# Kernel tuning notes

Hardware: AMD Instinct MI355X
Metric: run time of the kernel (lower is better)

The kernel has to match this reference:

```python
import jax, jax.numpy as jnp
import numpy as np

N_STATE = 64
SEQ_L = 4096
BATCH, HCH = 16, 512
DT_MIN, DT_MAX = 0.001, 0.1


def _make_DPLR_HiPPO(N):
    # HiPPO-LegS matrix and its NPLR -> DPLR decomposition (annotated-s4).
    P = np.sqrt(1 + 2 * np.arange(N))
    A = P[:, None] * P[None, :]
    A = np.tril(A) - np.diag(np.arange(N))
    nhippo = -A
    p = 0.5 * np.sqrt(2 * np.arange(1, N + 1) + 1.0)
    q = 2 * p
    S = nhippo + p[:, None] * q[None, :]
    Lambda, V = np.linalg.eig(S)
    Vc = V.conj().T
    p_t = Vc @ p
    q_t = Vc @ q.conj()
    return Lambda, p_t, q_t, Vc


def _ri(z):
    return np.stack([z.real, z.imag], axis=-1).astype(np.float32)


def setup_inputs() -> dict:
    key = jax.random.key(0)
    k_u, k_ct, k_b, k_d, k_ls = jax.random.split(key, 5)
    Lambda, p, q, Vc = _make_DPLR_HiPPO(N_STATE)
    u = jax.random.normal(k_u, (BATCH, HCH, SEQ_L), dtype=jnp.float32)
    # lecun_normal params (fan_in = N)
    Ct_ri = jax.random.normal(k_ct, (1, N_STATE, 2), dtype=jnp.float32) / np.sqrt(N_STATE)
    Bp = jax.random.normal(k_b, (N_STATE, 1), dtype=jnp.float32) / np.sqrt(N_STATE)
    D = jax.random.uniform(k_d, (1,), dtype=jnp.float32)
    log_step = jax.random.uniform(
        k_ls, (1,), dtype=jnp.float32,
        minval=np.log(DT_MIN), maxval=np.log(DT_MAX))
    return {
        "u": u,
        "Lambda_ri": jnp.asarray(_ri(Lambda)),
        "p_ri": jnp.asarray(_ri(p)),
        "q_ri": jnp.asarray(_ri(q)),
        "Vc_ri": jnp.asarray(_ri(Vc)),
        "Ct_ri": Ct_ri,
        "Bp": Bp,
        "D": D,
        "log_step": log_step,
    }


def _cplx(x_ri):
    return x_ri[..., 0] + 1j * x_ri[..., 1]


def _s4_kernel(Lambda, p, q, B, Ct, step, L):
    # DPLR generating function evaluated at the L roots of unity (K_gen_DPLR
    # + conv_from_gen), vectorized over frequencies.
    Omega = jnp.exp((-2j * jnp.pi) * (jnp.arange(L) / L))          # (L,)
    g = (2.0 / step) * ((1.0 - Omega) / (1.0 + Omega))             # (L,)
    c = 2.0 / (1.0 + Omega)                                        # (L,)
    denom = g[:, None] - Lambda[None, :]                           # (L, N)
    cauchy = lambda v: (v[None, :] / denom).sum(-1)                # (L,)
    k00 = cauchy(Ct.conj() * B)
    k01 = cauchy(Ct.conj() * p)
    k10 = cauchy(q.conj() * B)
    k11 = cauchy(q.conj() * p)
    at_roots = c * (k00 - k01 * (1.0 / (1.0 + k11)) * k10)
    return jnp.fft.ifft(at_roots, L).real                          # (L,)


def reference(u, Lambda_ri, p_ri, q_ri, Vc_ri, Ct_ri, Bp, D, log_step):
    L = u.shape[-1]
    Lambda = _cplx(Lambda_ri)
    p = _cplx(p_ri)
    q = _cplx(q_ri)
    Vc = _cplx(Vc_ri)
    Ct = _cplx(Ct_ri).reshape(-1)                  # (N,)
    B = (Vc @ Bp.astype(Vc.dtype)).reshape(-1)     # (N,) complex
    step = jnp.exp(log_step)[0]
    K = _s4_kernel(Lambda, p, q, B, Ct, step, L).astype(u.dtype)   # (L,)
    # non-circular convolution via zero-padded FFT along the last axis
    n = 2 * L
    y = jnp.fft.irfft(jnp.fft.rfft(u, n=n) * jnp.fft.rfft(K, n=n), n=n)[..., :L]
    return y + D[0] * u
```

## Files before the change

### kernel.cpp

```cpp
#include <hip/hip_runtime.h>
#include <math.h>


#define SEQ_L 4096
#define NFFT  8192
#define NST   64
#define NROWS 8192
#define TWO_PI 6.28318530717958647692f

typedef float2 cf;

__device__ __forceinline__ cf cmul(cf a, cf b){ return make_float2(a.x*b.x - a.y*b.y, a.x*b.y + a.y*b.x); }
__device__ __forceinline__ cf cadd(cf a, cf b){ return make_float2(a.x+b.x, a.y+b.y); }
__device__ __forceinline__ cf csub(cf a, cf b){ return make_float2(a.x-b.x, a.y-b.y); }
__device__ __forceinline__ double2 dcmul(double2 a, double2 b) {
  return make_double2(a.x*b.x - a.y*b.y, a.x*b.y + a.y*b.x);
}
__device__ __forceinline__ int sw(int p){ return p ^ ((p >> 4) & 15); }

template<int S>
__device__ __forceinline__ void r4(cf& a0, cf& a1, cf& a2, cf& a3){
  cf t0 = cadd(a0,a2), t1 = csub(a0,a2);
  cf t2 = cadd(a1,a3), t3 = csub(a1,a3);
  cf w = (S < 0) ? make_float2(t3.y, -t3.x) : make_float2(-t3.y, t3.x);
  a0 = cadd(t0,t2); a2 = csub(t0,t2);
  a1 = cadd(t1,w);  a3 = csub(t1,w);
}

template<int S, bool ZHI>
__device__ __forceinline__ void dft8(cf x[8]){
  const float C = 0.70710678118654752f;
  cf e0,e1,e2,e3,o0,o1,o2,o3;
  if (ZHI) {
    cf w  = (S<0)? make_float2(x[2].y,-x[2].x) : make_float2(-x[2].y,x[2].x);
    e0 = cadd(x[0],x[2]); e2 = csub(x[0],x[2]);
    e1 = cadd(x[0],w);    e3 = csub(x[0],w);
    cf w2 = (S<0)? make_float2(x[3].y,-x[3].x) : make_float2(-x[3].y,x[3].x);
    o0 = cadd(x[1],x[3]); o2 = csub(x[1],x[3]);
    o1 = cadd(x[1],w2);   o3 = csub(x[1],w2);
  } else {
    cf a0=x[0],a1=x[2],a2=x[4],a3=x[6];
    r4<S>(a0,a1,a2,a3);  e0=a0;e1=a1;e2=a2;e3=a3;
    cf b0=x[1],b1=x[3],b2=x[5],b3=x[7];
    r4<S>(b0,b1,b2,b3);  o0=b0;o1=b1;o2=b2;o3=b3;
  }
  x[0] = cadd(e0,o0); x[4] = csub(e0,o0);
  cf t1 = (S<0)? make_float2(C*(o1.x+o1.y), C*(o1.y-o1.x))
               : make_float2(C*(o1.x-o1.y), C*(o1.x+o1.y));
  x[1] = cadd(e1,t1); x[5] = csub(e1,t1);
  cf t2 = (S<0)? make_float2(o2.y,-o2.x) : make_float2(-o2.y,o2.x);
  x[2] = cadd(e2,t2); x[6] = csub(e2,t2);
  cf t3 = (S<0)? make_float2(C*(o3.y-o3.x), -C*(o3.x+o3.y))
               : make_float2(-C*(o3.x+o3.y), C*(o3.x-o3.y));
  x[3] = cadd(e3,t3); x[7] = csub(e3,t3);
}

__device__ __forceinline__ void chain8(cf x[8], float th){
  float sn, cs; __sincosf(th, &sn, &cs);
  cf w = make_float2(cs, sn), wk = w;
  x[1] = cmul(x[1], wk);
  #pragma unroll
  for (int k = 2; k < 8; ++k) { wk = cmul(wk, w); x[k] = cmul(x[k], wk); }
}

__device__ __forceinline__ constexpr float c16t(int d){
  return (d==1)?0.92387953251128675613f:(d==2)?0.70710678118654752440f:
         (d==3)?0.38268343236508977173f:(d==4)?0.f:
         (d==5)?-0.38268343236508977173f:(d==6)?-0.70710678118654752440f:
         -0.92387953251128675613f;
}
__device__ __forceinline__ constexpr float s16t(int d){
  return (d==1)?0.38268343236508977173f:(d==2)?0.70710678118654752440f:
         (d==3)?0.92387953251128675613f:(d==4)?1.f:
         (d==5)?0.92387953251128675613f:(d==6)?0.70710678118654752440f:
         0.38268343236508977173f;
}
template<int S>
__device__ __forceinline__ void tw16(cf x[8], int t000){
  #pragma unroll
  for (int d = 1; d < 8; ++d) {
    float ce = t000 ? c16t(d) : 1.f;
    float se = t000 ? ((S < 0) ? -s16t(d) : s16t(d)) : 0.f;
    cf a = x[d];
    x[d] = make_float2(a.x*ce - a.y*se, a.x*se + a.y*ce);
  }
}

__device__ __forceinline__ void r2_shfl(cf x[8], int tid){
  const float sgn = (tid & 1) ? -1.f : 1.f;
  #pragma unroll
  for (int k = 0; k < 8; ++k) {
    float ox = __shfl_xor(x[k].x, 1, 64);
    float oy = __shfl_xor(x[k].y, 1, 64);
    x[k].x = ox + sgn * x[k].x;
    x[k].y = oy + sgn * x[k].y;
  }
}

template<bool ZHI>
__device__ __forceinline__ void fwd_all(cf x[8], cf* lds, int tid){
  int a1 = tid >> 7, t0 = tid & 127, t00 = tid & 15;
  int b2 = (tid >> 4) & 7, c3 = (tid >> 1) & 7, t000 = tid & 1;
  dft8<-1, ZHI>(x);
  chain8(x, -TWO_PI * (float)tid / (float)NFFT);
  #pragma unroll
  for (int a = 0; a < 8; ++a) lds[sw(a*1024 + tid)] = x[a];
  __syncthreads();
  #pragma unroll
  for (int r = 0; r < 8; ++r) x[r] = lds[sw(a1*1024 + t0 + 128*r)];
  dft8<-1, false>(x);
  chain8(x, -TWO_PI * (float)t0 / 1024.f);
  __syncthreads();
  #pragma unroll
  for (int b = 0; b < 8; ++b) lds[sw(a1*1024 + b*128 + t0)] = x[b];
  __syncthreads();
  #pragma unroll
  for (int r = 0; r < 8; ++r) x[r] = lds[sw(a1*1024 + b2*128 + t00 + 16*r)];
  dft8<-1, false>(x);
  chain8(x, -TWO_PI * (float)t00 / 128.f);
  __syncthreads();
  #pragma unroll
  for (int c = 0; c < 8; ++c) lds[sw(a1*1024 + b2*128 + c*16 + t00)] = x[c];
  __syncthreads();
  #pragma unroll
  for (int r = 0; r < 8; ++r) x[r] = lds[sw(a1*1024 + b2*128 + c3*16 + t000 + 2*r)];
  dft8<-1, false>(x);
  tw16<-1>(x, t000);
  r2_shfl(x, tid);
}

__device__ __forceinline__ void inv_all(cf x[8], cf* lds, int tid){
  int a1 = tid >> 7, t0 = tid & 127, t00 = tid & 15;
  int b2 = (tid >> 4) & 7, c3 = (tid >> 1) & 7, t000 = tid & 1;
  r2_shfl(x, tid);
  tw16<1>(x, t000);
  dft8<1, false>(x);
  __syncthreads();
  #pragma unroll
  for (int r = 0; r < 8; ++r) lds[sw(a1*1024 + b2*128 + c3*16 + t000 + 2*r)] = x[r];
  __syncthreads();
  #pragma unroll
  for (int c = 0; c < 8; ++c) x[c] = lds[sw(a1*1024 + b2*128 + c*16 + t00)];
  chain8(x, TWO_PI * (float)t00 / 128.f);
  dft8<1, false>(x);
  __syncthreads();
  #pragma unroll
  for (int r = 0; r < 8; ++r) lds[sw(a1*1024 + b2*128 + t00 + 16*r)] = x[r];
  __syncthreads();
  #pragma unroll
  for (int b = 0; b < 8; ++b) x[b] = lds[sw(a1*1024 + b*128 + t0)];
  chain8(x, TWO_PI * (float)t0 / 1024.f);
  dft8<1, false>(x);
  __syncthreads();
  #pragma unroll
  for (int r = 0; r < 8; ++r) lds[sw(a1*1024 + t0 + 128*r)] = x[r];
  __syncthreads();
  #pragma unroll
  for (int a = 0; a < 8; ++a) x[a] = lds[sw(a*1024 + tid)];
  chain8(x, TWO_PI * (float)tid / (float)NFFT);
  dft8<1, false>(x);
}

__global__ __launch_bounds__(256) void k_at(
    const float* __restrict__ Lam_ri, const float* __restrict__ p_ri,
    const float* __restrict__ q_ri,  const float* __restrict__ Vc_ri,
    const float* __restrict__ Ct_ri, const float* __restrict__ Bp,
    const float* __restrict__ log_step, float2* __restrict__ atroots) {
  __shared__ double2 lam[NST], ctB[NST], ctp[NST], qB[NST], qp[NST];
  __shared__ double stepd;
  int tx = threadIdx.x;
  if (tx < NST) {
    int n = tx;
    double lr = Lam_ri[2*n], li = Lam_ri[2*n+1];
    double pr = p_ri[2*n],  pi = p_ri[2*n+1];
    double qr = q_ri[2*n],  qi = q_ri[2*n+1];
    double cr = Ct_ri[2*n], ci = Ct_ri[2*n+1];
    double br = 0.0, bi = 0.0;
    for (int m = 0; m < NST; ++m) {
      double b = (double)Bp[m];
      br += (double)Vc_ri[2*(n*NST+m)]   * b;
      bi += (double)Vc_ri[2*(n*NST+m)+1] * b;
    }
    lam[n] = make_double2(lr, li);
    ctB[n] = make_double2(cr*br + ci*bi, cr*bi - ci*br);
    ctp[n] = make_double2(cr*pr + ci*pi, cr*pi - ci*pr);
    qB[n]  = make_double2(qr*br + qi*bi, qr*bi - qi*br);
    qp[n]  = make_double2(qr*pr + qi*pi, qr*pi - qi*pr);
  }
  if (tx == 0) stepd = exp((double)log_step[0]);
  __syncthreads();
  int l = blockIdx.x * 256 + tx;
  double ang = -2.0 * M_PI * (double)l / (double)SEQ_L;
  double sn, cs;
  sincos(ang, &sn, &cs);
  double2 onem = make_double2(1.0 - cs, -sn);
  double2 onep = make_double2(1.0 + cs,  sn);
  double den = onep.x*onep.x + onep.y*onep.y;
  double2 ip = make_double2(onep.x/den, -onep.y/den);
  double2 g  = dcmul(onem, ip);
  double tw = 2.0 / stepd;
  g.x *= tw; g.y *= tw;
  double2 cc = make_double2(2.0*ip.x, 2.0*ip.y);
  double2 k00 = make_double2(0,0), k01 = make_double2(0,0);
  double2 k10 = make_double2(0,0), k11 = make_double2(0,0);
  for (int n = 0; n < NST; ++n) {
    double2 L = lam[n];
    double2 d = make_double2(g.x - L.x, g.y - L.y);
    double dd = d.x*d.x + d.y*d.y;
    double2 inv = make_double2(d.x/dd, -d.y/dd);
    double2 v;
    v = ctB[n]; k00.x += v.x*inv.x - v.y*inv.y; k00.y += v.x*inv.y + v.y*inv.x;
    v = ctp[n]; k01.x += v.x*inv.x - v.y*inv.y; k01.y += v.x*inv.y + v.y*inv.x;
    v = qB[n];  k10.x += v.x*inv.x - v.y*inv.y; k10.y += v.x*inv.y + v.y*inv.x;
    v = qp[n];  k11.x += v.x*inv.x - v.y*inv.y; k11.y += v.x*inv.y + v.y*inv.x;
  }
  double2 k11p = make_double2(1.0 + k11.x, k11.y);
  double2 num  = dcmul(k01, k10);
  double dd2 = k11p.x*k11p.x + k11p.y*k11p.y;
  double2 t = make_double2((num.x*k11p.x + num.y*k11p.y)/dd2,
                           (num.y*k11p.x - num.x*k11p.y)/dd2);
  double2 inner = make_double2(k00.x - t.x, k00.y - t.y);
  double2 at = dcmul(cc, inner);
  atroots[l] = make_float2((float)at.x, (float)at.y);
}

__global__ __launch_bounds__(512) void k_kt(const float2* __restrict__ atroots,
                                            float* __restrict__ Kt) {
  int gid  = blockIdx.x * 512 + threadIdx.x;
  int t    = gid >> 6;
  int lane = gid & 63;
  float acc = 0.f;
  for (int l = lane; l < SEQ_L; l += 64) {
    int ph = (l * t) & (SEQ_L - 1);
    float a = (float)ph * (TWO_PI / (float)SEQ_L);
    float sn, cs; __sincosf(a, &sn, &cs);
    float2 v = atroots[l];
    acc += v.x*cs - v.y*sn;
  }
  for (int off = 32; off > 0; off >>= 1) acc += __shfl_down(acc, off, 64);
  if (lane == 0) Kt[t] = acc * (1.0f / (float)SEQ_L);
}

__global__ __launch_bounds__(1024) void k_kf(const float* __restrict__ Kt,
                                             cf* __restrict__ kf) {
  __shared__ cf lds[NFFT];
  int tid = threadIdx.x;
  cf x[8];
  #pragma unroll
  for (int m = 0; m < 4; ++m) x[m] = make_float2(Kt[tid + 1024*m], 0.f);
  #pragma unroll
  for (int m = 4; m < 8; ++m) x[m] = make_float2(0.f, 0.f);
  fwd_all<true>(x, lds, tid);
  const float s = 1.f / (float)NFFT;
  #pragma unroll
  for (int d = 0; d < 8; ++d)
    kf[tid*8 + d] = make_float2(x[d].x * s, x[d].y * s);
}

__global__ __launch_bounds__(1024, 4) void k_conv(const float* __restrict__ u,
                                                  const cf* __restrict__ kf,
                                                  const float* __restrict__ Dp,
                                                  float* __restrict__ out) {
  __shared__ cf lds[NFFT];
  int tid = threadIdx.x;
  size_t row0 = (size_t)blockIdx.x * 2;
  const float* ru0 = u + row0 * SEQ_L;
  const float* ru1 = ru0 + SEQ_L;
  cf x[8];
  #pragma unroll
  for (int m = 0; m < 4; ++m) {
    int n = tid + 1024*m;
    x[m] = make_float2(ru0[n], ru1[n]);
  }
  #pragma unroll
  for (int m = 4; m < 8; ++m) x[m] = make_float2(0.f, 0.f);

  fwd_all<true>(x, lds, tid);

  const float4* kf4 = (const float4*)kf + (size_t)tid * 4;
  #pragma unroll
  for (int k = 0; k < 4; ++k) {
    float4 kk = kf4[k];
    x[2*k]   = cmul(x[2*k],   make_float2(kk.x, kk.y));
    x[2*k+1] = cmul(x[2*k+1], make_float2(kk.z, kk.w));
  }

  inv_all(x, lds, tid);

  float Dv = Dp[0];
  float* o0 = out + row0 * SEQ_L;
  float* o1 = o0 + SEQ_L;
  #pragma unroll
  for (int m = 0; m < 4; ++m) {
    int n = tid + 1024*m;
    o0[n] = x[m].x + Dv * ru0[n];
    o1[n] = x[m].y + Dv * ru1[n];
  }
}

extern "C" void kernel_launch(void* const* d_in, const int* in_sizes, int n_in,
                              void* d_out, int out_size, void* d_ws, size_t ws_size,
                              hipStream_t stream) {
  const float* u      = (const float*)d_in[0];
  const float* Lam_ri = (const float*)d_in[1];
  const float* p_ri   = (const float*)d_in[2];
  const float* q_ri   = (const float*)d_in[3];
  const float* Vc_ri  = (const float*)d_in[4];
  const float* Ct_ri  = (const float*)d_in[5];
  const float* Bp     = (const float*)d_in[6];
  const float* Dp     = (const float*)d_in[7];
  const float* ls     = (const float*)d_in[8];

  char* ws = (char*)d_ws;
  float2* atroots = (float2*)(ws);
  float*  Kt      = (float*) (ws + 32768);
  cf*     kf      = (cf*)    (ws + 49152);

  k_at<<<dim3(SEQ_L/256), dim3(256), 0, stream>>>(Lam_ri, p_ri, q_ri, Vc_ri, Ct_ri, Bp, ls, atroots);
  k_kt<<<dim3(512), dim3(512), 0, stream>>>(atroots, Kt);
  k_kf<<<dim3(1), dim3(1024), 0, stream>>>(Kt, kf);
  k_conv<<<dim3(NROWS/2), dim3(1024), 0, stream>>>(u, kf, Dp, (float*)d_out);
}
```

Baseline: 204.3 us.

## Convolve each real row via a half-length complex FFT with split post-processing

Replaces the two-rows-packed 8192-point complex FFT convolution with a per-row real-FFT trick. Each real row of 4096 samples is packed as 2048... actually as a 4096-point complex sequence, and the multiply is done in the half-spectrum domain using conjugate-pair (k, M-k) coefficients alpha/beta precomputed in new small kernels. The kernel FFT spectrum is built from even bins taken directly from atroots and odd bins from a direct DFT, which removes the single-block k_kf FFT. The FFT stages now use 512 threads with 8 blocks per CU and new LDS swizzles, and the last inverse radix-8 computes only the needed half. This adds an extra LDS round-trip for the mirrored bins and several tiny kernel launches.

```diff
diff --git a/kernel.cpp b/kernel.cpp
--- a/kernel.cpp
+++ b/kernel.cpp
@@ -3,6 +3,7 @@
 
 
 #define SEQ_L 4096
+#define M4    4096
 #define NFFT  8192
 #define NST   64
 #define NROWS 8192
@@ -16,7 +17,10 @@
 __device__ __forceinline__ double2 dcmul(double2 a, double2 b) {
   return make_double2(a.x*b.x - a.y*b.y, a.x*b.y + a.y*b.x);
 }
-__device__ __forceinline__ int sw(int p){ return p ^ ((p >> 4) & 15); }
+
+__device__ __forceinline__ int s2f(int i){ return i ^ (((i >> 6) & 1) << 3); }
+__device__ __forceinline__ int s3f(int i){ return i ^ ((i >> 6) & 7) ^ (((i >> 6) & 1) << 3); }
+__device__ __forceinline__ int smf(int i){ return i ^ ((i >> 6) & 7); }
 
 template<int S>
 __device__ __forceinline__ void r4(cf& a0, cf& a1, cf& a2, cf& a3){
@@ -27,7 +31,7 @@
   a1 = cadd(t1,w);  a3 = csub(t1,w);
 }
 
-template<int S, bool ZHI>
+template<int S, bool ZHI, bool LO4=false>
 __device__ __forceinline__ void dft8(cf x[8]){
   const float C = 0.70710678118654752f;
   cf e0,e1,e2,e3,o0,o1,o2,o3;
@@ -44,121 +48,29 @@
     cf b0=x[1],b1=x[3],b2=x[5],b3=x[7];
     r4<S>(b0,b1,b2,b3);  o0=b0;o1=b1;o2=b2;o3=b3;
   }
-  x[0] = cadd(e0,o0); x[4] = csub(e0,o0);
+  x[0] = cadd(e0,o0); if (!LO4) x[4] = csub(e0,o0);
   cf t1 = (S<0)? make_float2(C*(o1.x+o1.y), C*(o1.y-o1.x))
                : make_float2(C*(o1.x-o1.y), C*(o1.x+o1.y));
-  x[1] = cadd(e1,t1); x[5] = csub(e1,t1);
+  x[1] = cadd(e1,t1); if (!LO4) x[5] = csub(e1,t1);
   cf t2 = (S<0)? make_float2(o2.y,-o2.x) : make_float2(-o2.y,o2.x);
-  x[2] = cadd(e2,t2); x[6] = csub(e2,t2);
+  x[2] = cadd(e2,t2); if (!LO4) x[6] = csub(e2,t2);
   cf t3 = (S<0)? make_float2(C*(o3.y-o3.x), -C*(o3.x+o3.y))
                : make_float2(-C*(o3.x+o3.y), C*(o3.x-o3.y));
-  x[3] = cadd(e3,t3); x[7] = csub(e3,t3);
+  x[3] = cadd(e3,t3); if (!LO4) x[7] = csub(e3,t3);
 }
 
 __device__ __forceinline__ void chain8(cf x[8], float th){
   float sn, cs; __sincosf(th, &sn, &cs);
-  cf w = make_float2(cs, sn), wk = w;
-  x[1] = cmul(x[1], wk);
-  #pragma unroll
-  for (int k = 2; k < 8; ++k) { wk = cmul(wk, w); x[k] = cmul(x[k], wk); }
-}
-
-__device__ __forceinline__ constexpr float c16t(int d){
-  return (d==1)?0.92387953251128675613f:(d==2)?0.70710678118654752440f:
-         (d==3)?0.38268343236508977173f:(d==4)?0.f:
-         (d==5)?-0.38268343236508977173f:(d==6)?-0.70710678118654752440f:
-         -0.92387953251128675613f;
-}
-__device__ __forceinline__ constexpr float s16t(int d){
-  return (d==1)?0.38268343236508977173f:(d==2)?0.70710678118654752440f:
-         (d==3)?0.92387953251128675613f:(d==4)?1.f:
-         (d==5)?0.92387953251128675613f:(d==6)?0.70710678118654752440f:
-         0.38268343236508977173f;
-}
-template<int S>
-__device__ __forceinline__ void tw16(cf x[8], int t000){
-  #pragma unroll
-  for (int d = 1; d < 8; ++d) {
-    float ce = t000 ? c16t(d) : 1.f;
-    float se = t000 ? ((S < 0) ? -s16t(d) : s16t(d)) : 0.f;
-    cf a = x[d];
-    x[d] = make_float2(a.x*ce - a.y*se, a.x*se + a.y*ce);
-  }
-}
-
-__device__ __forceinline__ void r2_shfl(cf x[8], int tid){
-  const float sgn = (tid & 1) ? -1.f : 1.f;
-  #pragma unroll
-  for (int k = 0; k < 8; ++k) {
-    float ox = __shfl_xor(x[k].x, 1, 64);
-    float oy = __shfl_xor(x[k].y, 1, 64);
-    x[k].x = ox + sgn * x[k].x;
-    x[k].y = oy + sgn * x[k].y;
-  }
-}
-
-template<bool ZHI>
-__device__ __forceinline__ void fwd_all(cf x[8], cf* lds, int tid){
-  int a1 = tid >> 7, t0 = tid & 127, t00 = tid & 15;
-  int b2 = (tid >> 4) & 7, c3 = (tid >> 1) & 7, t000 = tid & 1;
-  dft8<-1, ZHI>(x);
-  chain8(x, -TWO_PI * (float)tid / (float)NFFT);
-  #pragma unroll
-  for (int a = 0; a < 8; ++a) lds[sw(a*1024 + tid)] = x[a];
-  __syncthreads();
-  #pragma unroll
-  for (int r = 0; r < 8; ++r) x[r] = lds[sw(a1*1024 + t0 + 128*r)];
-  dft8<-1, false>(x);
-  chain8(x, -TWO_PI * (float)t0 / 1024.f);
-  __syncthreads();
-  #pragma unroll
-  for (int b = 0; b < 8; ++b) lds[sw(a1*1024 + b*128 + t0)] = x[b];
-  __syncthreads();
-  #pragma unroll
-  for (int r = 0; r < 8; ++r) x[r] = lds[sw(a1*1024 + b2*128 + t00 + 16*r)];
-  dft8<-1, false>(x);
-  chain8(x, -TWO_PI * (float)t00 / 128.f);
-  __syncthreads();
-  #pragma unroll
-  for (int c = 0; c < 8; ++c) lds[sw(a1*1024 + b2*128 + c*16 + t00)] = x[c];
-  __syncthreads();
-  #pragma unroll
-  for (int r = 0; r < 8; ++r) x[r] = lds[sw(a1*1024 + b2*128 + c3*16 + t000 + 2*r)];
-  dft8<-1, false>(x);
-  tw16<-1>(x, t000);
-  r2_shfl(x, tid);
-}
-
-__device__ __forceinline__ void inv_all(cf x[8], cf* lds, int tid){
-  int a1 = tid >> 7, t0 = tid & 127, t00 = tid & 15;
-  int b2 = (tid >> 4) & 7, c3 = (tid >> 1) & 7, t000 = tid & 1;
-  r2_shfl(x, tid);
-  tw16<1>(x, t000);
-  dft8<1, false>(x);
-  __syncthreads();
-  #pragma unroll
-  for (int r = 0; r < 8; ++r) lds[sw(a1*1024 + b2*128 + c3*16 + t000 + 2*r)] = x[r];
-  __syncthreads();
-  #pragma unroll
-  for (int c = 0; c < 8; ++c) x[c] = lds[sw(a1*1024 + b2*128 + c*16 + t00)];
-  chain8(x, TWO_PI * (float)t00 / 128.f);
-  dft8<1, false>(x);
-  __syncthreads();
-  #pragma unroll
-  for (int r = 0; r < 8; ++r) lds[sw(a1*1024 + b2*128 + t00 + 16*r)] = x[r];
-  __syncthreads();
-  #pragma unroll
-  for (int b = 0; b < 8; ++b) x[b] = lds[sw(a1*1024 + b*128 + t0)];
-  chain8(x, TWO_PI * (float)t0 / 1024.f);
-  dft8<1, false>(x);
-  __syncthreads();
-  #pragma unroll
-  for (int r = 0; r < 8; ++r) lds[sw(a1*1024 + t0 + 128*r)] = x[r];
-  __syncthreads();
-  #pragma unroll
-  for (int a = 0; a < 8; ++a) x[a] = lds[sw(a*1024 + tid)];
-  chain8(x, TWO_PI * (float)tid / (float)NFFT);
-  dft8<1, false>(x);
+  cf w1 = make_float2(cs, sn);
+  cf w2 = cmul(w1, w1);
+  cf w3 = cmul(w2, w1);
+  cf w4 = cmul(w2, w2);
+  cf w5 = cmul(w3, w2);
+  cf w6 = cmul(w3, w3);
+  cf w7 = cmul(w4, w3);
+  x[1] = cmul(x[1], w1); x[2] = cmul(x[2], w2); x[3] = cmul(x[3], w3);
+  x[4] = cmul(x[4], w4); x[5] = cmul(x[5], w5); x[6] = cmul(x[6], w6);
+  x[7] = cmul(x[7], w7);
 }
 
 __global__ __launch_bounds__(256) void k_at(
@@ -241,60 +153,151 @@
   if (lane == 0) Kt[t] = acc * (1.0f / (float)SEQ_L);
 }
 
-__global__ __launch_bounds__(1024) void k_kf(const float* __restrict__ Kt,
-                                             cf* __restrict__ kf) {
-  __shared__ cf lds[NFFT];
-  int tid = threadIdx.x;
+__global__ __launch_bounds__(256) void k_geven(const float2* __restrict__ atroots,
+                                               float2* __restrict__ G) {
+  int l = blockIdx.x * 256 + threadIdx.x;
+  if (l > 2048) return;
+  float2 a = atroots[l];
+  float2 b = atroots[(M4 - l) & (M4 - 1)];
+  G[2*l] = make_float2(0.5f*(a.x + b.x), 0.5f*(a.y - b.y));
+}
+
+__global__ __launch_bounds__(512) void k_godd(const float* __restrict__ Kt,
+                                              float2* __restrict__ G) {
+  int gid  = blockIdx.x * 512 + threadIdx.x;
+  int w    = gid >> 6;
+  int k    = 2*w + 1;
+  int lane = gid & 63;
+  float ar = 0.f, ai = 0.f;
+  for (int t = lane; t < SEQ_L; t += 64) {
+    int ph = (k * t) & (NFFT - 1);
+    float a = (float)ph * (-TWO_PI / (float)NFFT);
+    float sn, cs; __sincosf(a, &sn, &cs);
+    float kv = Kt[t];
+    ar += kv * cs; ai += kv * sn;
+  }
+  for (int off = 32; off > 0; off >>= 1) {
+    ar += __shfl_down(ar, off, 64);
+    ai += __shfl_down(ai, off, 64);
+  }
+  if (lane == 0) G[k] = make_float2(ar, ai);
+}
+
+__global__ __launch_bounds__(256) void k_ab(const float2* __restrict__ G,
+                                            float4* __restrict__ ab) {
+  int idx = blockIdx.x * 256 + threadIdx.x;
+  int tidc = idx >> 3, d = idx & 7;
+  int k = (tidc >> 6) + 8*((tidc >> 3) & 7) + 64*(tidc & 7) + 512*d;
+  double ang = -2.0 * M_PI * (double)k / (double)NFFT;
+  double sn, cs; sincos(ang, &sn, &cs);
+  double2 a = make_double2(0.5*(1.0 + sn), -0.5*cs);
+  double2 b = make_double2(0.5*(1.0 - sn),  0.5*cs);
+  double2 p = make_double2(0.5*(1.0 + sn),  0.5*cs);
+  double2 q = make_double2(0.5*(1.0 - sn), -0.5*cs);
+  float2 gk = G[k];
+  float2 gh = G[M4 - k];
+  double2 Gk = make_double2(gk.x, gk.y);
+  double2 Gh = make_double2(gh.x, -gh.y);
+  double2 pa = dcmul(p, a), pb = dcmul(p, b);
+  double2 qa = dcmul(q, a), qb = dcmul(q, b);
+  double2 al = dcmul(pa, Gk), t1 = dcmul(qb, Gh);
+  al.x += t1.x; al.y += t1.y;
+  double2 be = dcmul(pb, Gk), t2 = dcmul(qa, Gh);
+  be.x += t2.x; be.y += t2.y;
+  const double s = 1.0 / (double)M4;
+  ab[idx] = make_float4((float)(al.x*s), (float)(al.y*s),
+                        (float)(be.x*s), (float)(be.y*s));
+}
+
+__global__ __launch_bounds__(512, 8) void k_conv(const float* __restrict__ u,
+                                                 const float4* __restrict__ ab,
+                                                 const float* __restrict__ Dp,
+                                                 float* __restrict__ out) {
+  __shared__ cf lds[M4];
+  const int tid = threadIdx.x;
+  const size_t row = blockIdx.x;
+  const float2* ru = (const float2*)(u + row * SEQ_L);
+  const int a1 = tid >> 6, t0 = tid & 63, b2 = (tid >> 3) & 7, t00 = tid & 7;
+
   cf x[8];
   #pragma unroll
-  for (int m = 0; m < 4; ++m) x[m] = make_float2(Kt[tid + 1024*m], 0.f);
+  for (int m = 0; m < 4; ++m) { float2 v = ru[tid + 512*m]; x[m] = make_float2(v.x, v.y); }
   #pragma unroll
   for (int m = 4; m < 8; ++m) x[m] = make_float2(0.f, 0.f);
-  fwd_all<true>(x, lds, tid);
-  const float s = 1.f / (float)NFFT;
-  #pragma unroll
-  for (int d = 0; d < 8; ++d)
-    kf[tid*8 + d] = make_float2(x[d].x * s, x[d].y * s);
-}
-
-__global__ __launch_bounds__(1024, 4) void k_conv(const float* __restrict__ u,
-                                                  const cf* __restrict__ kf,
-                                                  const float* __restrict__ Dp,
-                                                  float* __restrict__ out) {
-  __shared__ cf lds[NFFT];
-  int tid = threadIdx.x;
-  size_t row0 = (size_t)blockIdx.x * 2;
-  const float* ru0 = u + row0 * SEQ_L;
-  const float* ru1 = ru0 + SEQ_L;
-  cf x[8];
+
+  dft8<-1, true>(x);
+  chain8(x, -TWO_PI * (float)tid / (float)M4);
+  #pragma unroll
+  for (int a = 0; a < 8; ++a) lds[a*512 + tid] = x[a];
+  __syncthreads();
+  #pragma unroll
+  for (int r = 0; r < 8; ++r) x[r] = lds[a1*512 + t0 + 64*r];
+  dft8<-1, false>(x);
+  chain8(x, -TWO_PI * (float)t0 / 512.f);
+  __syncthreads();
+  #pragma unroll
+  for (int b = 0; b < 8; ++b) lds[s2f(a1*512 + b*64 + t0)] = x[b];
+  __syncthreads();
+  #pragma unroll
+  for (int r = 0; r < 8; ++r) x[r] = lds[s2f(a1*512 + b2*64 + t00 + 8*r)];
+  dft8<-1, false>(x);
+  chain8(x, -TWO_PI * (float)t00 / 64.f);
+  __syncthreads();
+  #pragma unroll
+  for (int c = 0; c < 8; ++c) lds[s3f(a1*512 + b2*64 + c*8 + t00)] = x[c];
+  __syncthreads();
+  #pragma unroll
+  for (int r = 0; r < 8; ++r) x[r] = lds[s3f(a1*512 + b2*64 + t00*8 + r)];
+  dft8<-1, false>(x);
+  __syncthreads();
+
+  const int base = a1 + 8*b2 + 64*t00;
+  #pragma unroll
+  for (int d = 0; d < 8; ++d) lds[smf(base + 512*d)] = x[d];
+  __syncthreads();
+  cf t[8];
+  #pragma unroll
+  for (int d = 0; d < 8; ++d) t[d] = lds[smf((M4 - base - 512*d) & (M4 - 1))];
+  const float4* abp = ab + (size_t)tid * 8;
+  #pragma unroll
+  for (int d = 0; d < 8; ++d) {
+    float4 c = abp[d];
+    x[d] = make_float2(c.x*x[d].x - c.y*x[d].y + c.z*t[d].x + c.w*t[d].y,
+                       c.x*x[d].y + c.y*x[d].x + c.w*t[d].x - c.z*t[d].y);
+  }
+  __syncthreads();
+
+  dft8<1, false>(x);
+  #pragma unroll
+  for (int r = 0; r < 8; ++r) lds[s3f(a1*512 + b2*64 + t00*8 + r)] = x[r];
+  __syncthreads();
+  #pragma unroll
+  for (int c = 0; c < 8; ++c) x[c] = lds[s3f(a1*512 + b2*64 + c*8 + t00)];
+  chain8(x, TWO_PI * (float)t00 / 64.f);
+  dft8<1, false>(x);
+  __syncthreads();
+  #pragma unroll
+  for (int r = 0; r < 8; ++r) lds[s2f(a1*512 + b2*64 + t00 + 8*r)] = x[r];
+  __syncthreads();
+  #pragma unroll
+  for (int b = 0; b < 8; ++b) x[b] = lds[s2f(a1*512 + b*64 + t0)];
+  chain8(x, TWO_PI * (float)t0 / 512.f);
+  dft8<1, false>(x);
+  __syncthreads();
+  #pragma unroll
+  for (int r = 0; r < 8; ++r) lds[a1*512 + t0 + 64*r] = x[r];
+  __syncthreads();
+  #pragma unroll
+  for (int a = 0; a < 8; ++a) x[a] = lds[a*512 + tid];
+  chain8(x, TWO_PI * (float)tid / (float)M4);
+  dft8<1, false, true>(x);
+
+  const float Dv = Dp[0];
+  float2* o = (float2*)(out + row * SEQ_L);
   #pragma unroll
   for (int m = 0; m < 4; ++m) {
-    int n = tid + 1024*m;
-    x[m] = make_float2(ru0[n], ru1[n]);
-  }
-  #pragma unroll
-  for (int m = 4; m < 8; ++m) x[m] = make_float2(0.f, 0.f);
-
-  fwd_all<true>(x, lds, tid);
-
-  const float4* kf4 = (const float4*)kf + (size_t)tid * 4;
-  #pragma unroll
-  for (int k = 0; k < 4; ++k) {
-    float4 kk = kf4[k];
-    x[2*k]   = cmul(x[2*k],   make_float2(kk.x, kk.y));
-    x[2*k+1] = cmul(x[2*k+1], make_float2(kk.z, kk.w));
-  }
-
-  inv_all(x, lds, tid);
-
-  float Dv = Dp[0];
-  float* o0 = out + row0 * SEQ_L;
-  float* o1 = o0 + SEQ_L;
-  #pragma unroll
-  for (int m = 0; m < 4; ++m) {
-    int n = tid + 1024*m;
-    o0[n] = x[m].x + Dv * ru0[n];
-    o1[n] = x[m].y + Dv * ru1[n];
+    float2 uv = ru[tid + 512*m];
+    o[tid + 512*m] = make_float2(x[m].x + Dv*uv.x, x[m].y + Dv*uv.y);
   }
 }
 
@@ -314,10 +317,13 @@
   char* ws = (char*)d_ws;
   float2* atroots = (float2*)(ws);
   float*  Kt      = (float*) (ws + 32768);
-  cf*     kf      = (cf*)    (ws + 49152);
-
-  k_at<<<dim3(SEQ_L/256), dim3(256), 0, stream>>>(Lam_ri, p_ri, q_ri, Vc_ri, Ct_ri, Bp, ls, atroots);
-  k_kt<<<dim3(512), dim3(512), 0, stream>>>(atroots, Kt);
-  k_kf<<<dim3(1), dim3(1024), 0, stream>>>(Kt, kf);
-  k_conv<<<dim3(NROWS/2), dim3(1024), 0, stream>>>(u, kf, Dp, (float*)d_out);
-}
+  float2* G       = (float2*)(ws + 49152);
+  float4* ab      = (float4*)(ws + 81936);
+
+  k_at   <<<dim3(SEQ_L/256), dim3(256), 0, stream>>>(Lam_ri, p_ri, q_ri, Vc_ri, Ct_ri, Bp, ls, atroots);
+  k_kt   <<<dim3(512),  dim3(512), 0, stream>>>(atroots, Kt);
+  k_geven<<<dim3(9),    dim3(256), 0, stream>>>(atroots, G);
+  k_godd <<<dim3(256),  dim3(512), 0, stream>>>(Kt, G);
+  k_ab   <<<dim3(16),   dim3(256), 0, stream>>>(G, ab);
+  k_conv <<<dim3(NROWS), dim3(512), 0, stream>>>(u, ab, Dp, (float*)d_out);
+}
```

Result: slower. 249.9 us (+22.4%).
